# Performance work log

Measured on AMD Instinct MI355X. Metric: run time of the kernel, lower is better.

## Reference

```python
import jax, jax.numpy as jnp
import numpy as np

N, E = 50000, 250000
SD, VM = 128, 64          # scalar channels, vector multiplicity (irreps: 128x0e + 64x1e)
EA, SH = 64, 4            # edge_attr dim, spherical-harmonics dim (1x0e + 1x1e)
H, FC = 16, 256
HD = FC // H              # head dim = 16
EPS = 1e-5


def _split(x):
    return x[:, :SD], x[:, SD:].reshape(-1, VM, 3)


def _ln(s, V):
    # equivariant layer norm: standardize scalars; RMS-normalize vector norms
    s = (s - s.mean(-1, keepdims=True)) * jax.lax.rsqrt(s.var(-1, keepdims=True) + EPS)
    vn = jax.lax.rsqrt(jnp.mean(jnp.sum(V * V, -1), -1, keepdims=True) + EPS)
    return s, V * vn[..., None]


def setup_inputs() -> dict:
    key = jax.random.key(0)
    ks = iter(jax.random.split(key, 48))
    rn = lambda shp, sc=1.0: jax.random.normal(next(ks), shp, dtype=jnp.float32) * sc
    w = lambda i, o: rn((i, o), 1.0 / np.sqrt(i))
    z = lambda d: jnp.zeros((d,), jnp.float32)
    return dict(
        node_features=rn((N, SD + 3 * VM)),
        edge_attr=rn((E, EA)),
        edge_sh=rn((E, SH)),
        Wq=w(SD, FC), bq=z(FC),
        Wk=w(SD, FC), bk=z(FC),
        We=w(EA, FC), be=z(FC),
        Wv_s=w(SD, SD), bv_s=z(SD), Wv_v=w(VM, VM),
        w_ss=w(SD, SD), w_vv_s=w(VM, SD), w_ssg=w(SD, VM), w_vvg=w(VM, VM),
        b_ms=z(SD), b_mg=z(VM),
        w_sv=w(SD, VM), w_vs=w(VM, VM), w_vvv=w(VM, VM),
        Wo_s=w(SD, SD), bo_s=z(SD), Wo_v=w(VM, VM),
        W1_s=w(SD, SD + VM), b1_s=z(SD + VM), W1_v=w(VM, VM),
        W2_s=w(SD, SD), b2_s=z(SD), W2_v=w(VM, VM),
        edge_index=jax.random.randint(next(ks), (2, E), 0, N, dtype=jnp.int32),
        batch=jnp.zeros((N,), jnp.int32),
    )


def reference(node_features, edge_attr, edge_sh, Wq, bq, Wk, bk, We, be,
              Wv_s, bv_s, Wv_v, w_ss, w_vv_s, w_ssg, w_vvg, b_ms, b_mg,
              w_sv, w_vs, w_vvv, Wo_s, bo_s, Wo_v,
              W1_s, b1_s, W1_v, W2_s, b2_s, W2_v, edge_index, batch):
    src, dst = edge_index[0], edge_index[1]
    ns, nV = _split(node_features)                        # [N,SD], [N,VM,3]

    # per-edge multi-head attention scores (gathered q/k + edge bias term)
    q = (ns[dst] @ Wq + bq).reshape(-1, H, HD)
    k = (ns[src] @ Wk + bk).reshape(-1, H, HD)
    ef = (edge_attr @ We + be).reshape(-1, H, HD)
    scores = ((q * k).sum(-1) + (q * ef).sum(-1)) / np.sqrt(HD)   # [E,H]

    # per-destination-node softmax (replaces the python unique(dst) loop)
    m = jax.ops.segment_max(scores, dst, num_segments=N)
    ex = jnp.exp(scores - m[dst])
    den = jax.ops.segment_sum(ex, dst, num_segments=N)
    attn = (ex / den[dst]).mean(-1, keepdims=True)                # [E,1]

    # v projection (o3.Linear) on source nodes
    vs = ns[src] @ Wv_s + bv_s                                    # [E,SD]
    Vv = jnp.einsum('evk,vu->euk', nV[src], Wv_v)                 # [E,VM,3]

    # message MLP: fully-connected tensor product with edge SH, norm, swish-gate
    shs, shv = edge_sh[:, 0], edge_sh[:, 1:4]
    s_in = vs * shs[:, None]                                      # 0e x 0e -> 0e
    dots = jnp.einsum('evk,ek->ev', Vv, shv)                      # 1e x 1e -> 0e
    ms = s_in @ w_ss + dots @ w_vv_s + b_ms                       # [E,SD] scalars
    mg = s_in @ w_ssg + dots @ w_vvg + b_mg                       # [E,VM] gates
    MV = ((vs @ w_sv)[:, :, None] * shv[:, None, :]               # 0e x 1e -> 1e
          + jnp.einsum('evk,vu->euk', Vv * shs[:, None, None], w_vs)   # 1e x 0e -> 1e
          + jnp.einsum('evk,vu->euk', jnp.cross(Vv, shv[:, None, :]), w_vvv))  # 1e x 1e -> 1e
    sg, MVn = _ln(jnp.concatenate([ms, mg], -1), MV)
    msg_s = jax.nn.silu(sg[:, :SD])
    msg_V = MVn * jax.nn.sigmoid(sg[:, SD:])[:, :, None]

    # attention-weighted scatter-sum aggregation to destination nodes
    agg_s = jax.ops.segment_sum(msg_s * attn, dst, num_segments=N)
    agg_V = jax.ops.segment_sum(msg_V * attn[:, :, None], dst, num_segments=N)

    # out projection + residual + norm1
    x_s = ns + (agg_s @ Wo_s + bo_s)
    x_V = nV + jnp.einsum('nvk,vu->nuk', agg_V, Wo_v)
    x_s, x_V = _ln(x_s, x_V)

    # gated equivariant FFN + residual + norm2
    f = x_s @ W1_s + b1_s                                         # [N,SD+VM]
    fV = jnp.einsum('nvk,vu->nuk', x_V, W1_v)
    gV = fV * jax.nn.sigmoid(f[:, SD:])[:, :, None]
    o_s = x_s + (jax.nn.silu(f[:, :SD]) @ W2_s + b2_s)
    o_V = x_V + jnp.einsum('nvk,vu->nuk', gV, W2_v)
    o_s, o_V = _ln(o_s, o_V)
    return jnp.concatenate([o_s, o_V.reshape(-1, 3 * VM)], -1)
```

## Files before the change

### kernel.cpp

```cpp
#include <hip/hip_runtime.h>
#include <hip/hip_bf16.h>

#define NNODE 50000
#define NEDGE 250000

typedef __hip_bfloat16 bf16;
typedef __attribute__((ext_vector_type(8))) short short8v;
typedef __attribute__((ext_vector_type(4))) float f32x4;

__device__ __forceinline__ float b2f(bf16 x){ return __bfloat162float(x); }
__device__ __forceinline__ bf16  f2b(float x){ return __float2bfloat16(x); }
__device__ __forceinline__ short f2s(float x){ bf16 h=f2b(x); short s; __builtin_memcpy(&s,&h,2); return s; }
__device__ __forceinline__ float s2f(short s){ bf16 h; __builtin_memcpy(&h,&s,2); return b2f(h); }
__device__ __forceinline__ float sigm(float x){ return 1.0f/(1.0f+__expf(-x)); }
__device__ __forceinline__ float wred64(float v){
  #pragma unroll
  for(int o=32;o>0;o>>=1) v+=__shfl_xor(v,o,64);
  return v;
}
__device__ __forceinline__ float gred16(float v){
  v+=__shfl_xor(v,1,64); v+=__shfl_xor(v,2,64); v+=__shfl_xor(v,4,64); v+=__shfl_xor(v,8,64);
  return v;
}
__device__ __forceinline__ int fragOff(int r, int k){
  int kt=k>>5, k32=k&31, half=k32>>4, g=(k32&15)>>2, j=k32&3;
  return (kt<<10)+((r+(g<<4))<<4)+(half<<3)+(j<<1);
}
__device__ __forceinline__ short8v pack8(float4 a, float4 b){
  short8v s; s[0]=f2s(a.x);s[1]=f2s(a.y);s[2]=f2s(a.z);s[3]=f2s(a.w);
  s[4]=f2s(b.x);s[5]=f2s(b.y);s[6]=f2s(b.z);s[7]=f2s(b.w); return s;
}
__device__ __forceinline__ short8v pack8s(short4 a, short4 b){
  short8v s; s[0]=a.x;s[1]=a.y;s[2]=a.z;s[3]=a.w;s[4]=b.x;s[5]=b.y;s[6]=b.z;s[7]=b.w; return s;
}

#define T_WOS 0
#define T_WOV 32
#define T_W1S 40
#define T_W1V 88
#define T_W2S 96
#define T_W2V 128
#define T_WE  136
#define T_WQ  168
#define T_WK  232
#define T_WVS 296
#define T_WSS 328
#define T_WSSG 360
#define T_WSV 376
#define T_WVV 392
#define T_WVVS 400
#define T_WVVG 416
#define T_WVS2 424
#define T_WVVV 432
#define T_TOT 440

__global__ __launch_bounds__(64) void k_prep(
  const float* __restrict__ Wo_s, const float* __restrict__ Wo_v,
  const float* __restrict__ W1_s, const float* __restrict__ W1_v,
  const float* __restrict__ W2_s, const float* __restrict__ W2_v,
  const float* __restrict__ WeM,
  const float* __restrict__ Wq, const float* __restrict__ Wk,
  const float* __restrict__ Wv_s,
  const float* __restrict__ w_ss, const float* __restrict__ w_ssg,
  const float* __restrict__ w_sv,
  const float* __restrict__ Wv_v, const float* __restrict__ w_vv_s,
  const float* __restrict__ w_vvg, const float* __restrict__ w_vs,
  const float* __restrict__ w_vvv,
  short* __restrict__ P)
{
  const int T=blockIdx.x, l=threadIdx.x;
  const float* W; int N, KT, lt;
  if(T<T_WOV){ W=Wo_s; N=128; KT=4; lt=T; }
  else if(T<T_W1S){ W=Wo_v; N=64; KT=2; lt=T-T_WOV; }
  else if(T<T_W1V){ W=W1_s; N=192; KT=4; lt=T-T_W1S; }
  else if(T<T_W2S){ W=W1_v; N=64; KT=2; lt=T-T_W1V; }
  else if(T<T_W2V){ W=W2_s; N=128; KT=4; lt=T-T_W2S; }
  else if(T<T_WE){ W=W2_v; N=64; KT=2; lt=T-T_W2V; }
  else if(T<T_WQ){ W=WeM; N=256; KT=2; lt=T-T_WE; }
  else if(T<T_WK){ W=Wq; N=256; KT=4; lt=T-T_WQ; }
  else if(T<T_WVS){ W=Wk; N=256; KT=4; lt=T-T_WK; }
  else if(T<T_WSS){ W=Wv_s; N=128; KT=4; lt=T-T_WVS; }
  else if(T<T_WSSG){ W=w_ss; N=128; KT=4; lt=T-T_WSS; }
  else if(T<T_WSV){ W=w_ssg; N=64; KT=4; lt=T-T_WSSG; }
  else if(T<T_WVV){ W=w_sv; N=64; KT=4; lt=T-T_WSV; }
  else if(T<T_WVVS){ W=Wv_v; N=64; KT=2; lt=T-T_WVV; }
  else if(T<T_WVVG){ W=w_vv_s; N=128; KT=2; lt=T-T_WVVS; }
  else if(T<T_WVS2){ W=w_vvg; N=64; KT=2; lt=T-T_WVVG; }
  else if(T<T_WVVV){ W=w_vs; N=64; KT=2; lt=T-T_WVS2; }
  else { W=w_vvv; N=64; KT=2; lt=T-T_WVVV; }
  const int nt=lt/KT, kt=lt-nt*KT;
  const int col=nt*16+(l&15);
  short8v o;
  #pragma unroll
  for(int j=0;j<8;j++){
    int k=kt*32+((j>>2)<<4)+((l>>4)<<2)+(j&3);
    o[j]=f2s(W[(size_t)k*N+col]);
  }
  *(short8v*)(P+((size_t)T<<9)+(l<<3))=o;
}


__global__ __launch_bounds__(256) void k1_mfma(
  const float* __restrict__ nf, const short* __restrict__ P,
  const float* __restrict__ bq, const float* __restrict__ bk,
  const float* __restrict__ bvs,
  bf16* __restrict__ Q, bf16* __restrict__ K, short* __restrict__ NREC2)
{
  __shared__ __align__(16) short nsF[4*512];
  __shared__ __align__(16) short vsF[4*512];
  const int t=threadIdx.x, l=t&63, w=t>>6;
  const int n0=blockIdx.x*16;
  for(int i=t;i<512;i+=256){
    int r=i>>5, c=(i&31)<<2;
    const float4 v=*(const float4*)&nf[(size_t)(n0+r)*320+c];
    short4 s; s.x=f2s(v.x); s.y=f2s(v.y); s.z=f2s(v.z); s.w=f2s(v.w);
    *(short4*)((char*)nsF+fragOff(r,c))=s;
  }
  __syncthreads();
  short8v a[4];
  #pragma unroll
  for(int kt=0;kt<4;kt++) a[kt]=*(const short8v*)((const char*)nsF+(kt<<10)+(l<<4));
  #pragma unroll
  for(int ii=0;ii<4;ii++){
    int nt=w+(ii<<2);
    f32x4 accq={0.f,0.f,0.f,0.f}, acck={0.f,0.f,0.f,0.f};
    #pragma unroll
    for(int kt=0;kt<4;kt++){
      short8v bq8=*(const short8v*)(P+(((size_t)(T_WQ+nt*4+kt))<<9)+(l<<3));
      short8v bk8=*(const short8v*)(P+(((size_t)(T_WK+nt*4+kt))<<9)+(l<<3));
      accq=__builtin_amdgcn_mfma_f32_16x16x32_bf16(a[kt],bq8,accq,0,0,0);
      acck=__builtin_amdgcn_mfma_f32_16x16x32_bf16(a[kt],bk8,acck,0,0,0);
    }
    int col=(nt<<4)+(l&15);
    float bqs=bq[col], bks=bk[col];
    #pragma unroll
    for(int r=0;r<4;r++){
      int row=((l>>4)<<2)+r;
      Q[(size_t)(n0+row)*256+col]=f2b(accq[r]+bqs);
      K[(size_t)(n0+row)*256+col]=f2b(acck[r]+bks);
    }
  }
  #pragma unroll
  for(int ii=0;ii<2;ii++){
    int nt=w+(ii<<2);
    f32x4 acc={0.f,0.f,0.f,0.f};
    #pragma unroll
    for(int kt=0;kt<4;kt++){
      short8v b=*(const short8v*)(P+(((size_t)(T_WVS+nt*4+kt))<<9)+(l<<3));
      acc=__builtin_amdgcn_mfma_f32_16x16x32_bf16(a[kt],b,acc,0,0,0);
    }
    int col=(nt<<4)+(l&15);
    float bv=bvs[col];
    #pragma unroll
    for(int r=0;r<4;r++){
      int row=((l>>4)<<2)+r;
      *(short*)((char*)vsF+fragOff(row,col))=f2s(acc[r]+bv);
    }
  }
  __syncthreads();
  #pragma unroll
  for(int kt=0;kt<4;kt++) a[kt]=*(const short8v*)((const char*)vsF+(kt<<10)+(l<<4));
  #pragma unroll
  for(int ii=0;ii<4;ii++){
    int nt=w+(ii<<2);
    int bt;
    if(nt<8) bt=T_WSS+nt*4;
    else if(nt<12) bt=T_WSSG+(nt-8)*4;
    else bt=T_WSV+(nt-12)*4;
    f32x4 acc={0.f,0.f,0.f,0.f};
    #pragma unroll
    for(int kt=0;kt<4;kt++){
      short8v b=*(const short8v*)(P+(((size_t)(bt+kt))<<9)+(l<<3));
      acc=__builtin_amdgcn_mfma_f32_16x16x32_bf16(a[kt],b,acc,0,0,0);
    }
    int col=(nt<<4)+(l&15);
    int lane, sslot;
    if(nt<8){ lane=col&63; sslot=(col>=64)?1:0; }
    else if(nt<12){ lane=col-128; sslot=2; }
    else { lane=col-192; sslot=3; }
    #pragma unroll
    for(int r=0;r<4;r++){
      int row=((l>>4)<<2)+r;
      NREC2[(size_t)(n0+row)*1280 + (lane<<2) + sslot]=f2s(acc[r]);
    }
  }
}

__global__ __launch_bounds__(256) void k2_mfma(
  const float* __restrict__ nf, const short* __restrict__ P,
  short* __restrict__ NREC2)
{
  __shared__ __align__(16) short nvF[6*512];
  __shared__ __align__(16) short vvF[6*512];
  const int t=threadIdx.x, l=t&63, w=t>>6;
  const int n0=blockIdx.x*16;
  for(int i=t;i<3072;i+=256){
    int r=i/192, c=i-r*192;
    int v=c/3, k=c-3*v;
    float x=nf[(size_t)(n0+r)*320+128+c];
    *(short*)((char*)nvF+(k<<11)+fragOff(r,v))=f2s(x);
  }
  __syncthreads();
  #pragma unroll
  for(int jj=0;jj<3;jj++){
    int job=w+(jj<<2);
    int p=job>>2, nt=job&3;
    f32x4 acc={0.f,0.f,0.f,0.f};
    #pragma unroll
    for(int kt=0;kt<2;kt++){
      short8v a2=*(const short8v*)((const char*)nvF+(p<<11)+(kt<<10)+(l<<4));
      short8v b=*(const short8v*)(P+(((size_t)(T_WVV+nt*2+kt))<<9)+(l<<3));
      acc=__builtin_amdgcn_mfma_f32_16x16x32_bf16(a2,b,acc,0,0,0);
    }
    int col=(nt<<4)+(l&15);
    #pragma unroll
    for(int r=0;r<4;r++){
      int row=((l>>4)<<2)+r;
      *(short*)((char*)vvF+(p<<11)+fragOff(row,col))=f2s(acc[r]);
    }
  }
  __syncthreads();
  #pragma unroll
  for(int jj=0;jj<15;jj++){
    int job=w+(jj<<2);
    int p=job/20, r20=job-p*20;
    int nt, bt, G0;
    if(r20<8){ nt=r20; bt=T_WVVS+nt*2; G0=0; }
    else if(r20<12){ nt=r20-8; bt=T_WVVG+nt*2; G0=1; }
    else if(r20<16){ nt=r20-12; bt=T_WVS2+nt*2; G0=2; }
    else { nt=r20-16; bt=T_WVVV+nt*2; G0=3; }
    f32x4 acc={0.f,0.f,0.f,0.f};
    #pragma unroll
    for(int kt=0;kt<2;kt++){
      short8v a2=*(const short8v*)((const char*)vvF+(p<<11)+(kt<<10)+(l<<4));
      short8v b=*(const short8v*)(P+(((size_t)(bt+kt))<<9)+(l<<3));
      acc=__builtin_amdgcn_mfma_f32_16x16x32_bf16(a2,b,acc,0,0,0);
    }
    int col=(nt<<4)+(l&15);
    int G;
    if(G0==0)      G = p*2 + (col>=64 ? 1 : 0);
    else if(G0==1) G = 6 + p;
    else if(G0==2) G = 9 + p;
    else           G = 12 + p;
    int lane = col & 63;
    int addr = ((1+(G>>2))<<8) + (lane<<2) + (G&3);
    #pragma unroll
    for(int r=0;r<4;r++){
      int row=((l>>4)<<2)+r;
      NREC2[(size_t)(n0+row)*1280 + addr]=f2s(acc[r]);
    }
  }
}

__global__ __launch_bounds__(256) void k_hist(const int* __restrict__ eidx, int* __restrict__ counts){
  int e=blockIdx.x*256+threadIdx.x;
  if(e<NEDGE) atomicAdd(&counts[eidx[NEDGE+e]],1);
}

__global__ __launch_bounds__(1024) void k_scan(const int* __restrict__ counts, int* __restrict__ off, int* __restrict__ cursor){
  __shared__ int wsum[16];
  __shared__ int woff[17];
  __shared__ int carry_s;
  const int t=threadIdx.x, ln=t&63, wid=t>>6;
  if(t==0) carry_s=0;
  __syncthreads();
  for(int base=0;base<NNODE;base+=1024){
    int idx=base+t;
    int v=(idx<NNODE)?counts[idx]:0;
    int incl=v;
    #pragma unroll
    for(int o=1;o<64;o<<=1){ int x=__shfl_up(incl,o,64); if(ln>=o) incl+=x; }
    if(ln==63) wsum[wid]=incl;
    __syncthreads();
    if(t<16){
      int s=wsum[t];
      #pragma unroll
      for(int o=1;o<16;o<<=1){ int x=__shfl_up(s,o,64); if(t>=o) s+=x; }
      woff[t+1]=s;
      if(t==0) woff[0]=0;
    }
    __syncthreads();
    int excl=carry_s+woff[wid]+(incl-v);
    if(idx<NNODE){ off[idx]=excl; cursor[idx]=excl; }
    __syncthreads();
    if(t==0) carry_s+=woff[16];
    __syncthreads();
  }
  if(t==0) off[NNODE]=NEDGE;
}

__global__ __launch_bounds__(256) void k_scatter(const int* __restrict__ eidx, int* __restrict__ cursor, int* __restrict__ eord){
  int e=blockIdx.x*256+threadIdx.x;
  if(e<NEDGE){
    int d=eidx[NEDGE+e];
    int pos=atomicAdd(&cursor[d],1);
    eord[pos]=e;
  }
}

__global__ __launch_bounds__(256) void k3_mfma(
  const float* __restrict__ eattr, const int* __restrict__ eidx,
  const short* __restrict__ P, const float* __restrict__ be,
  const bf16* __restrict__ Q, const bf16* __restrict__ K,
  float* __restrict__ SC)
{
  __shared__ __align__(16) short aeF[2*512];
  __shared__ __align__(16) float ef[16][260];
  __shared__ int ssrc[16], sdst[16];
  const int t=threadIdx.x, l=t&63, w=t>>6;
  const int e0=blockIdx.x*16;
  if(t<16){ ssrc[t]=eidx[e0+t]; sdst[t]=eidx[NEDGE+e0+t]; }
  {
    int r=t>>4, c4=(t&15)<<2;
    const float4 v=*(const float4*)&eattr[(size_t)(e0+r)*64+c4];
    short4 s; s.x=f2s(v.x); s.y=f2s(v.y); s.z=f2s(v.z); s.w=f2s(v.w);
    *(short4*)((char*)aeF+fragOff(r,c4))=s;
  }
  __syncthreads();
  {
    short8v a0=*(const short8v*)((const char*)aeF+(l<<4));
    short8v a1=*(const short8v*)((const char*)aeF+1024+(l<<4));
    #pragma unroll
    for(int ii=0;ii<4;ii++){
      int nt=w+(ii<<2);
      f32x4 acc={0.f,0.f,0.f,0.f};
      short8v b0=*(const short8v*)(P+(((size_t)(T_WE+nt*2+0))<<9)+(l<<3));
      short8v b1=*(const short8v*)(P+(((size_t)(T_WE+nt*2+1))<<9)+(l<<3));
      acc=__builtin_amdgcn_mfma_f32_16x16x32_bf16(a0,b0,acc,0,0,0);
      acc=__builtin_amdgcn_mfma_f32_16x16x32_bf16(a1,b1,acc,0,0,0);
      int col=(nt<<4)+(l&15);
      float bv=be[col];
      #pragma unroll
      for(int r=0;r<4;r++){ int row=((l>>4)<<2)+r; ef[row][col]=acc[r]+bv; }
    }
  }
  __syncthreads();
  {
    const int h=l&15, qt=l>>4;
    const int ch=h*16+(qt<<2);
    #pragma unroll
    for(int j=0;j<4;j++){
      int el=w*4+j;
      int s=ssrc[el], d=sdst[el];
      short4 qs=*(const short4*)((const short*)Q+(size_t)d*256+ch);
      short4 ks=*(const short4*)((const short*)K+(size_t)s*256+ch);
      const float4 e4=*(const float4*)&ef[el][ch];
      float p = s2f(qs.x)*(s2f(ks.x)+e4.x)
              + s2f(qs.y)*(s2f(ks.y)+e4.y)
              + s2f(qs.z)*(s2f(ks.z)+e4.z)
              + s2f(qs.w)*(s2f(ks.w)+e4.w);
      p += __shfl_xor(p,16,64);
      p += __shfl_xor(p,32,64);
      if(qt==0) SC[(size_t)(e0+el)*16+h]=p*0.25f;
    }
  }
}

__global__ __launch_bounds__(256) void k5_att(
  const float* __restrict__ SC, const int* __restrict__ OFF,
  const int* __restrict__ EORD, float* __restrict__ ATT)
{
  const int l=threadIdx.x&63;
  const int n=blockIdx.x*4+(threadIdx.x>>6);
  const int beg=OFF[n], end=OFF[n+1];
  const int j=l>>4, h=l&15;
  float mh=-1e30f;
  for(int i=beg+j;i<end;i+=4) mh=fmaxf(mh, SC[(size_t)EORD[i]*16+h]);
  mh=fmaxf(mh,__shfl_xor(mh,16,64));
  mh=fmaxf(mh,__shfl_xor(mh,32,64));
  float dh=0.f;
  for(int i=beg+j;i<end;i+=4) dh+=__expf(SC[(size_t)EORD[i]*16+h]-mh);
  dh+=__shfl_xor(dh,16,64);
  dh+=__shfl_xor(dh,32,64);
  float rdh=(end>beg)?1.f/dh:0.f;
  for(int i0=beg;i0<end;i0+=4){
    int i=i0+j;
    int e=0; float a=0.f; bool act=(i<end);
    if(act){ e=EORD[i]; a=__expf(SC[(size_t)e*16+h]-mh)*rdh; }
    a=gred16(a);
    if(h==0 && act) ATT[e]=a*(1.f/16.f);
  }
}

__global__ __launch_bounds__(256) void k6_agg(
  const int* __restrict__ eidx, const float* __restrict__ esh,
  const short* __restrict__ NREC2, const float* __restrict__ ATT,
  const int* __restrict__ OFF, const int* __restrict__ EORD,
  const float* __restrict__ b_ms, const float* __restrict__ b_mg,
  float* __restrict__ AGS, float* __restrict__ AGV)
{
  const int l = threadIdx.x & 63;
  const int n = blockIdx.x*4 + (threadIdx.x>>6);
  const int beg=OFF[n], end=OFF[n+1];
  const float bmsa=b_ms[l], bmsb=b_ms[64+l], bmgv=b_mg[l];

  float as0=0.f,as1=0.f,av0acc=0.f,av1acc=0.f,av2acc=0.f;
  for(int i=beg;i<end;i++){
    const int e=EORD[i];
    const int s=eidx[e];
    const float att=ATT[e];
    const float4 sh4=*(const float4*)&esh[(size_t)e*4];
    const float shs=sh4.x, sh0=sh4.y, sh1=sh4.z, sh2=sh4.w;

    const short* R = NREC2 + (size_t)s*1280 + (l<<2);
    const short4 q0=*(const short4*)(R);
    const short4 q1=*(const short4*)(R+256);
    const short4 q2=*(const short4*)(R+512);
    const short4 q3=*(const short4*)(R+768);
    const short4 q4=*(const short4*)(R+1024);

    float msa = shs*s2f(q0.x) + s2f(q1.x)*sh0 + s2f(q1.z)*sh1 + s2f(q2.x)*sh2 + bmsa;
    float msb = shs*s2f(q0.y) + s2f(q1.y)*sh0 + s2f(q1.w)*sh1 + s2f(q2.y)*sh2 + bmsb;
    float mgv = shs*s2f(q0.z) + s2f(q2.z)*sh0 + s2f(q2.w)*sh1 + s2f(q3.x)*sh2 + bmgv;

    float sum = wred64(msa+msb+mgv);
    float sq  = wred64(msa*msa+msb*msb+mgv*mgv);
    float mean = sum*(1.f/192.f);
    float var  = sq*(1.f/192.f) - mean*mean;
    float rs   = rsqrtf(var + 1e-5f);

    const float svv=s2f(q0.w);
    const float w0=s2f(q3.y), w1=s2f(q3.z), w2=s2f(q3.w);
    const float c0=s2f(q4.x), c1=s2f(q4.y), c2=s2f(q4.z);
    float cr0 = c1*sh2 - c2*sh1;
    float cr1 = c2*sh0 - c0*sh2;
    float cr2 = c0*sh1 - c1*sh0;
    float mv0 = svv*sh0 + shs*w0 + cr0;
    float mv1 = svv*sh1 + shs*w1 + cr1;
    float mv2 = svv*sh2 + shs*w2 + cr2;
    float vsq = wred64(mv0*mv0+mv1*mv1+mv2*mv2);
    float vn  = rsqrtf(vsq*(1.f/64.f) + 1e-5f);

    float sga=(msa-mean)*rs, sgb=(msb-mean)*rs, sgg=(mgv-mean)*rs;
    float wV = vn * sigm(sgg) * att;
    as0 += sga*sigm(sga)*att;
    as1 += sgb*sigm(sgb)*att;
    av0acc += mv0*wV;
    av1acc += mv1*wV;
    av2acc += mv2*wV;
  }
  AGS[(size_t)n*128+l]     =as0;
  AGS[(size_t)n*128+64+l]  =as1;
  AGV[(size_t)n*192+l]     =av0acc;
  AGV[(size_t)n*192+64+l]  =av1acc;
  AGV[(size_t)n*192+128+l] =av2acc;
}

__global__ __launch_bounds__(256) void k7_mfma(
  const float* __restrict__ nf,
  const float* __restrict__ AGS, const float* __restrict__ AGV,
  const short* __restrict__ P,
  const float* __restrict__ bo_s, const float* __restrict__ b1_s, const float* __restrict__ b2_s,
  float* __restrict__ out)
{
  __shared__ float xs[16][132];
  __shared__ float xv[16][196];
  __shared__ short ffh[16][204];
  __shared__ __align__(16) short asA[4*512];
  __shared__ __align__(16) short avA[6*512];
  __shared__ float smean[16], srs[16], svn[16];
  const int t=threadIdx.x, l=t&63, w=t>>6;
  const int n0=blockIdx.x*16;
  const int lam=t&63, kt4=t>>6;
  const int fr=lam&15, fg=lam>>4;

  for(int i=t;i<2048;i+=256){ int r=i>>7,c=i&127; xs[r][c]=nf[(size_t)(n0+r)*320+c]; }
  for(int i=t;i<3072;i+=256){ int r=i/192,cc=i-r*192; int k=cc>>6,u=cc&63; xv[r][cc]=nf[(size_t)(n0+r)*320+128+u*3+k]; }
  {
    const float* base=&AGS[(size_t)(n0+fr)*128 + (kt4<<5) + (fg<<2)];
    float4 va=*(const float4*)base, vb=*(const float4*)(base+16);
    *(short8v*)((char*)asA+(kt4<<10)+(lam<<4))=pack8(va,vb);
  }
  for(int i=t;i<384;i+=256){
    int seg=i>>6, lm=i&63, r=lm&15, g=lm>>4;
    int p=seg>>1, k2=seg&1;
    const float* base=&AGV[(size_t)(n0+r)*192 + (p<<6) + (k2<<5) + (g<<2)];
    float4 va=*(const float4*)base, vb=*(const float4*)(base+16);
    *(short8v*)((char*)avA+(seg<<10)+(lm<<4))=pack8(va,vb);
  }
  __syncthreads();

  {
    short8v a[4];
    #pragma unroll
    for(int kt=0;kt<4;kt++) a[kt]=*(const short8v*)((const char*)asA+(kt<<10)+(l<<4));
    #pragma unroll
    for(int ii=0;ii<2;ii++){
      int nt=w+(ii<<2);
      f32x4 acc={0.f,0.f,0.f,0.f};
      #pragma unroll
      for(int kt=0;kt<4;kt++){
        short8v b=*(const short8v*)(P+(((size_t)(T_WOS+nt*4+kt))<<9)+(l<<3));
        acc=__builtin_amdgcn_mfma_f32_16x16x32_bf16(a[kt],b,acc,0,0,0);
      }
      int col=(nt<<4)+(l&15);
      float bv=bo_s[col];
      #pragma unroll
      for(int r=0;r<4;r++){ int row=((l>>4)<<2)+r; xs[row][col]+=acc[r]+bv; }
    }
    #pragma unroll
    for(int ii=0;ii<3;ii++){
      int tid=w*3+ii, p=tid>>2, nt2=tid&3;
      f32x4 acc={0.f,0.f,0.f,0.f};
      #pragma unroll
      for(int kt=0;kt<2;kt++){
        short8v a2=*(const short8v*)((const char*)avA+(((p<<1)+kt)<<10)+(l<<4));
        short8v b=*(const short8v*)(P+(((size_t)(T_WOV+nt2*2+kt))<<9)+(l<<3));
        acc=__builtin_amdgcn_mfma_f32_16x16x32_bf16(a2,b,acc,0,0,0);
      }
      int col=(p<<6)+(nt2<<4)+(l&15);
      #pragma unroll
      for(int r=0;r<4;r++){ int row=((l>>4)<<2)+r; xv[row][col]+=acc[r]; }
    }
  }
  __syncthreads();

  {
    const int nn=t>>4, g=t&15;
    float sum=0,sq=0;
    #pragma unroll
    for(int j=0;j<8;j++){ float x=xs[nn][g+16*j]; sum+=x; sq+=x*x; }
    sum=gred16(sum); sq=gred16(sq);
    float mean=sum*(1.f/128.f);
    float var=sq*(1.f/128.f)-mean*mean;
    float vsq=0;
    #pragma unroll
    for(int j=0;j<12;j++){ float x=xv[nn][g+16*j]; vsq+=x*x; }
    vsq=gred16(vsq);
    if(g==0){ smean[nn]=mean; srs[nn]=rsqrtf(var+1e-5f); svn[nn]=rsqrtf(vsq*(1.f/64.f)+1e-5f); }
  }
  __syncthreads();

  for(int i=t;i<512;i+=256){
    int r=i>>5, c=(i&31)<<2;
    float m=smean[r], rs=srs[r];
    float4 v=*(float4*)&xs[r][c];
    v.x=(v.x-m)*rs; v.y=(v.y-m)*rs; v.z=(v.z-m)*rs; v.w=(v.w-m)*rs;
    *(float4*)&xs[r][c]=v;
  }
  for(int i=t;i<768;i+=256){
    int r=i/48, c=(i-r*48)<<2;
    float vn=svn[r];
    float4 v=*(float4*)&xv[r][c];
    v.x*=vn; v.y*=vn; v.z*=vn; v.w*=vn;
    *(float4*)&xv[r][c]=v;
  }
  __syncthreads();
  {
    float4 va=*(const float4*)&xs[fr][(kt4<<5)+(fg<<2)];
    float4 vb=*(const float4*)&xs[fr][(kt4<<5)+16+(fg<<2)];
    *(short8v*)((char*)asA+(kt4<<10)+(lam<<4))=pack8(va,vb);
  }
  for(int i=t;i<384;i+=256){
    int seg=i>>6, lm=i&63, r=lm&15, g=lm>>4;
    int p=seg>>1, k2=seg&1;
    float4 va=*(const float4*)&xv[r][(p<<6)+(k2<<5)+(g<<2)];
    float4 vb=*(const float4*)&xv[r][(p<<6)+(k2<<5)+16+(g<<2)];
    *(short8v*)((char*)avA+(seg<<10)+(lm<<4))=pack8(va,vb);
  }
  __syncthreads();

  {
    short8v a[4];
    #pragma unroll
    for(int kt=0;kt<4;kt++) a[kt]=*(const short8v*)((const char*)asA+(kt<<10)+(l<<4));
    #pragma unroll
    for(int ii=0;ii<3;ii++){
      int nt=w+(ii<<2);
      f32x4 acc={0.f,0.f,0.f,0.f};
      #pragma unroll
      for(int kt=0;kt<4;kt++){
        short8v b=*(const short8v*)(P+(((size_t)(T_W1S+nt*4+kt))<<9)+(l<<3));
        acc=__builtin_amdgcn_mfma_f32_16x16x32_bf16(a[kt],b,acc,0,0,0);
      }
      int col=(nt<<4)+(l&15);
      float bv=b1_s[col];
      #pragma unroll
      for(int r=0;r<4;r++){ int row=((l>>4)<<2)+r; ffh[row][col]=f2s(acc[r]+bv); }
    }
  }
  __syncthreads();

  f32x4 g4acc[3];
  {
    #pragma unroll
    for(int ii=0;ii<3;ii++){
      int tid=w*3+ii, p=tid>>2, nt2=tid&3;
      f32x4 acc={0.f,0.f,0.f,0.f};
      #pragma unroll
      for(int kt=0;kt<2;kt++){
        short8v a2=*(const short8v*)((const char*)avA+(((p<<1)+kt)<<10)+(l<<4));
        short8v b=*(const short8v*)(P+(((size_t)(T_W1V+nt2*2+kt))<<9)+(l<<3));
        acc=__builtin_amdgcn_mfma_f32_16x16x32_bf16(a2,b,acc,0,0,0);
      }
      g4acc[ii]=acc;
    }
    for(int i=t;i<512;i+=256){
      int r=i>>5, c=(i&31)<<2;
      short4 sv4=*(short4*)&ffh[r][c];
      float x0=s2f(sv4.x), x1=s2f(sv4.y), x2=s2f(sv4.z), x3=s2f(sv4.w);
      sv4.x=f2s(x0*sigm(x0)); sv4.y=f2s(x1*sigm(x1)); sv4.z=f2s(x2*sigm(x2)); sv4.w=f2s(x3*sigm(x3));
      *(short4*)&ffh[r][c]=sv4;
    }
  }
  __syncthreads();

  {
    short4 sa=*(const short4*)&ffh[fr][(kt4<<5)+(fg<<2)];
    short4 sb=*(const short4*)&ffh[fr][(kt4<<5)+16+(fg<<2)];
    *(short8v*)((char*)asA+(kt4<<10)+(lam<<4))=pack8s(sa,sb);
  }
  {
    #pragma unroll
    for(int ii=0;ii<3;ii++){
      int tid=w*3+ii, nt2=tid&3;
      int uu=(nt2<<4)+(l&15);
      #pragma unroll
      for(int r=0;r<4;r++){
        int row=((l>>4)<<2)+r;
        g4acc[ii][r]*=sigm(s2f(ffh[row][128+uu]));
      }
    }
  }
  __syncthreads();

  {
    #pragma unroll
    for(int ii=0;ii<3;ii++){
      int tid=w*3+ii, p=tid>>2, nt2=tid&3;
      int uu=(nt2<<4)+(l&15);
      #pragma unroll
      for(int r=0;r<4;r++){
        int row=((l>>4)<<2)+r;
        ffh[row][(p<<6)+uu]=f2s(g4acc[ii][r]);
      }
    }
  }
  __syncthreads();
  for(int i=t;i<384;i+=256){
    int seg=i>>6, lm=i&63, r=lm&15, g=lm>>4;
    int p=seg>>1, k2=seg&1;
    short4 sa=*(const short4*)&ffh[r][(p<<6)+(k2<<5)+(g<<2)];
    short4 sb=*(const short4*)&ffh[r][(p<<6)+(k2<<5)+16+(g<<2)];
    *(short8v*)((char*)avA+(seg<<10)+(lm<<4))=pack8s(sa,sb);
  }
  __syncthreads();

  {
    short8v a[4];
    #pragma unroll
    for(int kt=0;kt<4;kt++) a[kt]=*(const short8v*)((const char*)asA+(kt<<10)+(l<<4));
    #pragma unroll
    for(int ii=0;ii<2;ii++){
      int nt=w+(ii<<2);
      f32x4 acc={0.f,0.f,0.f,0.f};
      #pragma unroll
      for(int kt=0;kt<4;kt++){
        short8v b=*(const short8v*)(P+(((size_t)(T_W2S+nt*4+kt))<<9)+(l<<3));
        acc=__builtin_amdgcn_mfma_f32_16x16x32_bf16(a[kt],b,acc,0,0,0);
      }
      int col=(nt<<4)+(l&15);
      float bv=b2_s[col];
      #pragma unroll
      for(int r=0;r<4;r++){ int row=((l>>4)<<2)+r; xs[row][col]+=acc[r]+bv; }
    }
    #pragma unroll
    for(int ii=0;ii<3;ii++){
      int tid=w*3+ii, p=tid>>2, nt2=tid&3;
      f32x4 acc={0.f,0.f,0.f,0.f};
      #pragma unroll
      for(int kt=0;kt<2;kt++){
        short8v a2=*(const short8v*)((const char*)avA+(((p<<1)+kt)<<10)+(l<<4));
        short8v b=*(const short8v*)(P+(((size_t)(T_W2V+nt2*2+kt))<<9)+(l<<3));
        acc=__builtin_amdgcn_mfma_f32_16x16x32_bf16(a2,b,acc,0,0,0);
      }
      int col=(p<<6)+(nt2<<4)+(l&15);
      #pragma unroll
      for(int r=0;r<4;r++){ int row=((l>>4)<<2)+r; xv[row][col]+=acc[r]; }
    }
  }
  __syncthreads();

  {
    const int nn=t>>4, g=t&15;
    float sum=0,sq=0;
    #pragma unroll
    for(int j=0;j<8;j++){ float x=xs[nn][g+16*j]; sum+=x; sq+=x*x; }
    sum=gred16(sum); sq=gred16(sq);
    float mean=sum*(1.f/128.f);
    float var=sq*(1.f/128.f)-mean*mean;
    float vsq=0;
    #pragma unroll
    for(int j=0;j<12;j++){ float x=xv[nn][g+16*j]; vsq+=x*x; }
    vsq=gred16(vsq);
    if(g==0){ smean[nn]=mean; srs[nn]=rsqrtf(var+1e-5f); svn[nn]=rsqrtf(vsq*(1.f/64.f)+1e-5f); }
  }
  __syncthreads();

  for(int i=t;i<16*320;i+=256){
    int nn=i/320, c=i-nn*320;
    float v;
    if(c<128) v=(xs[nn][c]-smean[nn])*srs[nn];
    else { int j=c-128; int u=j/3, k=j-u*3; v=xv[nn][(k<<6)+u]*svn[nn]; }
    out[(size_t)(n0+nn)*320+c]=v;
  }
}

extern "C" void kernel_launch(void* const* d_in, const int* in_sizes, int n_in,
                              void* d_out, int out_size, void* d_ws, size_t ws_size,
                              hipStream_t stream)
{
  (void)in_sizes; (void)n_in; (void)out_size; (void)ws_size;
  const float* nf    =(const float*)d_in[0];
  const float* eattr =(const float*)d_in[1];
  const float* esh   =(const float*)d_in[2];
  const float* Wq    =(const float*)d_in[3];  const float* bq  =(const float*)d_in[4];
  const float* Wk    =(const float*)d_in[5];  const float* bk  =(const float*)d_in[6];
  const float* We    =(const float*)d_in[7];  const float* be  =(const float*)d_in[8];
  const float* Wv_s  =(const float*)d_in[9];  const float* bv_s=(const float*)d_in[10];
  const float* Wv_v  =(const float*)d_in[11];
  const float* w_ss  =(const float*)d_in[12]; const float* w_vv_s=(const float*)d_in[13];
  const float* w_ssg =(const float*)d_in[14]; const float* w_vvg =(const float*)d_in[15];
  const float* b_ms  =(const float*)d_in[16]; const float* b_mg  =(const float*)d_in[17];
  const float* w_sv  =(const float*)d_in[18]; const float* w_vs  =(const float*)d_in[19];
  const float* w_vvv =(const float*)d_in[20];
  const float* Wo_s  =(const float*)d_in[21]; const float* bo_s  =(const float*)d_in[22];
  const float* Wo_v  =(const float*)d_in[23];
  const float* W1_s  =(const float*)d_in[24]; const float* b1_s  =(const float*)d_in[25];
  const float* W1_v  =(const float*)d_in[26];
  const float* W2_s  =(const float*)d_in[27]; const float* b2_s  =(const float*)d_in[28];
  const float* W2_v  =(const float*)d_in[29];
  const int*   eidx  =(const int*)d_in[30];
  float* out=(float*)d_out;

  char* w=(char*)d_ws;
  bf16* Q    =(bf16*)w;  w+=(size_t)NNODE*256*2;
  bf16* Kb   =(bf16*)w;  w+=(size_t)NNODE*256*2;
  short* NREC2=(short*)w; w+=(size_t)NNODE*1280*2;
  float* SC  =(float*)w; w+=(size_t)NEDGE*16*4;
  float* ATT =(float*)w; w+=(size_t)NEDGE*4;
  float* AGS =(float*)w; w+=(size_t)NNODE*128*4;
  float* AGV =(float*)w; w+=(size_t)NNODE*192*4;
  short* P   =(short*)w; w+=(size_t)T_TOT*512*2;
  int* COUNTS=(int*)w;   w+=(size_t)NNODE*4;
  int* OFFb  =(int*)w;   w+=(size_t)(NNODE+1)*4;
  int* CURSOR=(int*)w;   w+=(size_t)NNODE*4;
  int* EORDb =(int*)w;   w+=(size_t)NEDGE*4;

  hipMemsetAsync(COUNTS,0,(size_t)NNODE*4,stream);

  k_prep    <<<T_TOT,64,0,stream>>>(Wo_s,Wo_v,W1_s,W1_v,W2_s,W2_v,We,
                                    Wq,Wk,Wv_s,w_ss,w_ssg,w_sv,
                                    Wv_v,w_vv_s,w_vvg,w_vs,w_vvv,P);
  k_hist    <<<(NEDGE+255)/256,256,0,stream>>>(eidx,COUNTS);
  k_scan    <<<1,1024,0,stream>>>(COUNTS,OFFb,CURSOR);
  k_scatter <<<(NEDGE+255)/256,256,0,stream>>>(eidx,CURSOR,EORDb);
  k1_mfma   <<<NNODE/16,256,0,stream>>>(nf,P,bq,bk,bv_s,Q,Kb,NREC2);
  k2_mfma   <<<NNODE/16,256,0,stream>>>(nf,P,NREC2);
  k3_mfma   <<<NEDGE/16,256,0,stream>>>(eattr,eidx,P,be,Q,Kb,SC);
  k5_att    <<<NNODE/4,256,0,stream>>>(SC,OFFb,EORDb,ATT);
  k6_agg    <<<NNODE/4,256,0,stream>>>(eidx,esh,NREC2,ATT,OFFb,EORDb,b_ms,b_mg,AGS,AGV);
  k7_mfma   <<<NNODE/16,256,0,stream>>>(nf,AGS,AGV,P,bo_s,b1_s,b2_s,out);
}
```

Baseline: 513.2 us.

## Fuse softmax into aggregation, fold histogram into edge-score kernel, prefetch gathers

The destination-degree histogram moves into the edge-score kernel, which removes the separate k_hist launch. The softmax normalisation is fused into the aggregation kernel: per-edge attention weights are computed in chunks of 64 into shared memory, so the ATT buffer and the k5 launch go away. The aggregation loop also software-prefetches the next edge's gathered node record and spherical harmonics to hide gather latency. The cost is higher register pressure and more sequential work inside each wave.

```diff
diff --git a/kernel.cpp b/kernel.cpp
--- a/kernel.cpp
+++ b/kernel.cpp
@@ -252,11 +252,6 @@
   }
 }
 
-__global__ __launch_bounds__(256) void k_hist(const int* __restrict__ eidx, int* __restrict__ counts){
-  int e=blockIdx.x*256+threadIdx.x;
-  if(e<NEDGE) atomicAdd(&counts[eidx[NEDGE+e]],1);
-}
-
 __global__ __launch_bounds__(1024) void k_scan(const int* __restrict__ counts, int* __restrict__ off, int* __restrict__ cursor){
   __shared__ int wsum[16];
   __shared__ int woff[17];
@@ -302,14 +297,19 @@
   const float* __restrict__ eattr, const int* __restrict__ eidx,
   const short* __restrict__ P, const float* __restrict__ be,
   const bf16* __restrict__ Q, const bf16* __restrict__ K,
-  float* __restrict__ SC)
+  float* __restrict__ SC, int* __restrict__ counts)
 {
   __shared__ __align__(16) short aeF[2*512];
   __shared__ __align__(16) float ef[16][260];
   __shared__ int ssrc[16], sdst[16];
   const int t=threadIdx.x, l=t&63, w=t>>6;
   const int e0=blockIdx.x*16;
-  if(t<16){ ssrc[t]=eidx[e0+t]; sdst[t]=eidx[NEDGE+e0+t]; }
+  if(t<16){
+    ssrc[t]=eidx[e0+t];
+    int d=eidx[NEDGE+e0+t];
+    sdst[t]=d;
+    atomicAdd(&counts[d],1);
+  }
   {
     int r=t>>4, c4=(t&15)<<2;
     const float4 v=*(const float4*)&eattr[(size_t)(e0+r)*64+c4];
@@ -356,14 +356,21 @@
   }
 }
 
-__global__ __launch_bounds__(256) void k5_att(
-  const float* __restrict__ SC, const int* __restrict__ OFF,
-  const int* __restrict__ EORD, float* __restrict__ ATT)
+__global__ __launch_bounds__(256) void k6_agg(
+  const int* __restrict__ eidx, const float* __restrict__ esh,
+  const short* __restrict__ NREC2, const float* __restrict__ SC,
+  const int* __restrict__ OFF, const int* __restrict__ EORD,
+  const float* __restrict__ b_ms, const float* __restrict__ b_mg,
+  float* __restrict__ AGS, float* __restrict__ AGV)
 {
-  const int l=threadIdx.x&63;
-  const int n=blockIdx.x*4+(threadIdx.x>>6);
+  __shared__ float att_s[4][64];
+  const int l = threadIdx.x & 63;
+  const int wid = threadIdx.x>>6;
+  const int n = blockIdx.x*4 + wid;
   const int beg=OFF[n], end=OFF[n+1];
+  const float bmsa=b_ms[l], bmsb=b_ms[64+l], bmgv=b_mg[l];
   const int j=l>>4, h=l&15;
+
   float mh=-1e30f;
   for(int i=beg+j;i<end;i+=4) mh=fmaxf(mh, SC[(size_t)EORD[i]*16+h]);
   mh=fmaxf(mh,__shfl_xor(mh,16,64));
@@ -372,72 +379,69 @@
   for(int i=beg+j;i<end;i+=4) dh+=__expf(SC[(size_t)EORD[i]*16+h]-mh);
   dh+=__shfl_xor(dh,16,64);
   dh+=__shfl_xor(dh,32,64);
-  float rdh=(end>beg)?1.f/dh:0.f;
-  for(int i0=beg;i0<end;i0+=4){
-    int i=i0+j;
-    int e=0; float a=0.f; bool act=(i<end);
-    if(act){ e=EORD[i]; a=__expf(SC[(size_t)e*16+h]-mh)*rdh; }
-    a=gred16(a);
-    if(h==0 && act) ATT[e]=a*(1.f/16.f);
-  }
-}
-
-__global__ __launch_bounds__(256) void k6_agg(
-  const int* __restrict__ eidx, const float* __restrict__ esh,
-  const short* __restrict__ NREC2, const float* __restrict__ ATT,
-  const int* __restrict__ OFF, const int* __restrict__ EORD,
-  const float* __restrict__ b_ms, const float* __restrict__ b_mg,
-  float* __restrict__ AGS, float* __restrict__ AGV)
-{
-  const int l = threadIdx.x & 63;
-  const int n = blockIdx.x*4 + (threadIdx.x>>6);
-  const int beg=OFF[n], end=OFF[n+1];
-  const float bmsa=b_ms[l], bmsb=b_ms[64+l], bmgv=b_mg[l];
+  const float rdh=(end>beg)?1.f/dh:0.f;
 
   float as0=0.f,as1=0.f,av0acc=0.f,av1acc=0.f,av2acc=0.f;
-  for(int i=beg;i<end;i++){
-    const int e=EORD[i];
-    const int s=eidx[e];
-    const float att=ATT[e];
-    const float4 sh4=*(const float4*)&esh[(size_t)e*4];
-    const float shs=sh4.x, sh0=sh4.y, sh1=sh4.z, sh2=sh4.w;
-
-    const short* R = NREC2 + (size_t)s*1280 + (l<<2);
-    const short4 q0=*(const short4*)(R);
-    const short4 q1=*(const short4*)(R+256);
-    const short4 q2=*(const short4*)(R+512);
-    const short4 q3=*(const short4*)(R+768);
-    const short4 q4=*(const short4*)(R+1024);
-
-    float msa = shs*s2f(q0.x) + s2f(q1.x)*sh0 + s2f(q1.z)*sh1 + s2f(q2.x)*sh2 + bmsa;
-    float msb = shs*s2f(q0.y) + s2f(q1.y)*sh0 + s2f(q1.w)*sh1 + s2f(q2.y)*sh2 + bmsb;
-    float mgv = shs*s2f(q0.z) + s2f(q2.z)*sh0 + s2f(q2.w)*sh1 + s2f(q3.x)*sh2 + bmgv;
-
-    float sum = wred64(msa+msb+mgv);
-    float sq  = wred64(msa*msa+msb*msb+mgv*mgv);
-    float mean = sum*(1.f/192.f);
-    float var  = sq*(1.f/192.f) - mean*mean;
-    float rs   = rsqrtf(var + 1e-5f);
-
-    const float svv=s2f(q0.w);
-    const float w0=s2f(q3.y), w1=s2f(q3.z), w2=s2f(q3.w);
-    const float c0=s2f(q4.x), c1=s2f(q4.y), c2=s2f(q4.z);
-    float cr0 = c1*sh2 - c2*sh1;
-    float cr1 = c2*sh0 - c0*sh2;
-    float cr2 = c0*sh1 - c1*sh0;
-    float mv0 = svv*sh0 + shs*w0 + cr0;
-    float mv1 = svv*sh1 + shs*w1 + cr1;
-    float mv2 = svv*sh2 + shs*w2 + cr2;
-    float vsq = wred64(mv0*mv0+mv1*mv1+mv2*mv2);
-    float vn  = rsqrtf(vsq*(1.f/64.f) + 1e-5f);
-
-    float sga=(msa-mean)*rs, sgb=(msb-mean)*rs, sgg=(mgv-mean)*rs;
-    float wV = vn * sigm(sgg) * att;
-    as0 += sga*sigm(sga)*att;
-    as1 += sgb*sigm(sgb)*att;
-    av0acc += mv0*wV;
-    av1acc += mv1*wV;
-    av2acc += mv2*wV;
+
+  for(int cb=beg; cb<end; cb+=64){
+    const int ce = (cb+64<end)? cb+64 : end;
+    for(int i0=cb;i0<ce;i0+=4){
+      int i=i0+j; bool act=(i<ce);
+      float a = act ? __expf(SC[(size_t)EORD[i]*16+h]-mh)*rdh : 0.f;
+      a=gred16(a);
+      if(h==0&&act) att_s[wid][i-cb]=a*(1.f/16.f);
+    }
+    int e=EORD[cb], s=eidx[e];
+    const short* R=NREC2+(size_t)s*1280+(l<<2);
+    short4 q0=*(const short4*)(R),     q1=*(const short4*)(R+256);
+    short4 q2=*(const short4*)(R+512), q3=*(const short4*)(R+768);
+    short4 q4=*(const short4*)(R+1024);
+    float4 sh4=*(const float4*)&esh[(size_t)e*4];
+
+    for(int i=cb;i<ce;i++){
+      const short4 p0=q0,p1=q1,p2=q2,p3=q3,p4=q4;
+      const float4 ps=sh4;
+      if(i+1<ce){
+        int e2=EORD[i+1], s2=eidx[e2];
+        const short* R2=NREC2+(size_t)s2*1280+(l<<2);
+        q0=*(const short4*)(R2);     q1=*(const short4*)(R2+256);
+        q2=*(const short4*)(R2+512); q3=*(const short4*)(R2+768);
+        q4=*(const short4*)(R2+1024);
+        sh4=*(const float4*)&esh[(size_t)e2*4];
+      }
+      const float att=att_s[wid][i-cb];
+      const float shs=ps.x, sh0=ps.y, sh1=ps.z, sh2=ps.w;
+
+      float msa = shs*s2f(p0.x) + s2f(p1.x)*sh0 + s2f(p1.z)*sh1 + s2f(p2.x)*sh2 + bmsa;
+      float msb = shs*s2f(p0.y) + s2f(p1.y)*sh0 + s2f(p1.w)*sh1 + s2f(p2.y)*sh2 + bmsb;
+      float mgv = shs*s2f(p0.z) + s2f(p2.z)*sh0 + s2f(p2.w)*sh1 + s2f(p3.x)*sh2 + bmgv;
+
+      float sum = wred64(msa+msb+mgv);
+      float sq  = wred64(msa*msa+msb*msb+mgv*mgv);
+      float mean = sum*(1.f/192.f);
+      float var  = sq*(1.f/192.f) - mean*mean;
+      float rs   = rsqrtf(var + 1e-5f);
+
+      const float svv=s2f(p0.w);
+      const float w0=s2f(p3.y), w1=s2f(p3.z), w2=s2f(p3.w);
+      const float c0=s2f(p4.x), c1=s2f(p4.y), c2=s2f(p4.z);
+      float cr0 = c1*sh2 - c2*sh1;
+      float cr1 = c2*sh0 - c0*sh2;
+      float cr2 = c0*sh1 - c1*sh0;
+      float mv0 = svv*sh0 + shs*w0 + cr0;
+      float mv1 = svv*sh1 + shs*w1 + cr1;
+      float mv2 = svv*sh2 + shs*w2 + cr2;
+      float vsq = wred64(mv0*mv0+mv1*mv1+mv2*mv2);
+      float vn  = rsqrtf(vsq*(1.f/64.f) + 1e-5f);
+
+      float sga=(msa-mean)*rs, sgb=(msb-mean)*rs, sgg=(mgv-mean)*rs;
+      float wV = vn * sigm(sgg) * att;
+      as0 += sga*sigm(sga)*att;
+      as1 += sgb*sigm(sgb)*att;
+      av0acc += mv0*wV;
+      av1acc += mv1*wV;
+      av2acc += mv2*wV;
+    }
   }
   AGS[(size_t)n*128+l]     =as0;
   AGS[(size_t)n*128+64+l]  =as1;
@@ -738,7 +742,6 @@
   bf16* Kb   =(bf16*)w;  w+=(size_t)NNODE*256*2;
   short* NREC2=(short*)w; w+=(size_t)NNODE*1280*2;
   float* SC  =(float*)w; w+=(size_t)NEDGE*16*4;
-  float* ATT =(float*)w; w+=(size_t)NEDGE*4;
   float* AGS =(float*)w; w+=(size_t)NNODE*128*4;
   float* AGV =(float*)w; w+=(size_t)NNODE*192*4;
   short* P   =(short*)w; w+=(size_t)T_TOT*512*2;
@@ -752,13 +755,11 @@
   k_prep    <<<T_TOT,64,0,stream>>>(Wo_s,Wo_v,W1_s,W1_v,W2_s,W2_v,We,
                                     Wq,Wk,Wv_s,w_ss,w_ssg,w_sv,
                                     Wv_v,w_vv_s,w_vvg,w_vs,w_vvv,P);
-  k_hist    <<<(NEDGE+255)/256,256,0,stream>>>(eidx,COUNTS);
+  k1_mfma   <<<NNODE/16,256,0,stream>>>(nf,P,bq,bk,bv_s,Q,Kb,NREC2);
+  k2_mfma   <<<NNODE/16,256,0,stream>>>(nf,P,NREC2);
+  k3_mfma   <<<NEDGE/16,256,0,stream>>>(eattr,eidx,P,be,Q,Kb,SC,COUNTS);
   k_scan    <<<1,1024,0,stream>>>(COUNTS,OFFb,CURSOR);
   k_scatter <<<(NEDGE+255)/256,256,0,stream>>>(eidx,CURSOR,EORDb);
-  k1_mfma   <<<NNODE/16,256,0,stream>>>(nf,P,bq,bk,bv_s,Q,Kb,NREC2);
-  k2_mfma   <<<NNODE/16,256,0,stream>>>(nf,P,NREC2);
-  k3_mfma   <<<NEDGE/16,256,0,stream>>>(eattr,eidx,P,be,Q,Kb,SC);
-  k5_att    <<<NNODE/4,256,0,stream>>>(SC,OFFb,EORDb,ATT);
-  k6_agg    <<<NNODE/4,256,0,stream>>>(eidx,esh,NREC2,ATT,OFFb,EORDb,b_ms,b_mg,AGS,AGV);
+  k6_agg    <<<NNODE/4,256,0,stream>>>(eidx,esh,NREC2,SC,OFFb,EORDb,b_ms,b_mg,AGS,AGV);
   k7_mfma   <<<NNODE/16,256,0,stream>>>(nf,AGS,AGV,P,bo_s,b1_s,b2_s,out);
 }
```

New measurement: 542.8 us. 1.06x slower.

## Parallelize CSR scan, fuse histogram into k3, and store edge data in sorted order

Applied to the files above, without the earlier changes.

The single-block serial scan over 50000 nodes becomes a three-kernel multi-block scan. The destination histogram moves into k3's edge loop, so the separate k_hist pass disappears. k_scatter now also writes source ids and spherical harmonics in destination-sorted order, and k5 writes attention in sorted order. This lets k6 read contiguously instead of doing indirect EORD gathers. The cost is extra workspace, two more small launches, and additional scatter writes.

```diff
diff --git a/kernel.cpp b/kernel.cpp
--- a/kernel.cpp
+++ b/kernel.cpp
@@ -20,6 +20,11 @@
 }
 __device__ __forceinline__ float gred16(float v){
   v+=__shfl_xor(v,1,64); v+=__shfl_xor(v,2,64); v+=__shfl_xor(v,4,64); v+=__shfl_xor(v,8,64);
+  return v;
+}
+__device__ __forceinline__ int ired64(int v){
+  #pragma unroll
+  for(int o=32;o>0;o>>=1) v+=__shfl_xor(v,o,64);
   return v;
 }
 __device__ __forceinline__ int fragOff(int r, int k){
@@ -252,49 +257,64 @@
   }
 }
 
-__global__ __launch_bounds__(256) void k_hist(const int* __restrict__ eidx, int* __restrict__ counts){
-  int e=blockIdx.x*256+threadIdx.x;
-  if(e<NEDGE) atomicAdd(&counts[eidx[NEDGE+e]],1);
-}
-
-__global__ __launch_bounds__(1024) void k_scan(const int* __restrict__ counts, int* __restrict__ off, int* __restrict__ cursor){
-  __shared__ int wsum[16];
-  __shared__ int woff[17];
-  __shared__ int carry_s;
+#define SCAN_NB 196
+
+__global__ __launch_bounds__(256) void k_scan1(const int* __restrict__ counts, int* __restrict__ bsum){
   const int t=threadIdx.x, ln=t&63, wid=t>>6;
-  if(t==0) carry_s=0;
-  __syncthreads();
-  for(int base=0;base<NNODE;base+=1024){
-    int idx=base+t;
-    int v=(idx<NNODE)?counts[idx]:0;
-    int incl=v;
-    #pragma unroll
-    for(int o=1;o<64;o<<=1){ int x=__shfl_up(incl,o,64); if(ln>=o) incl+=x; }
-    if(ln==63) wsum[wid]=incl;
-    __syncthreads();
-    if(t<16){
-      int s=wsum[t];
-      #pragma unroll
-      for(int o=1;o<16;o<<=1){ int x=__shfl_up(s,o,64); if(t>=o) s+=x; }
-      woff[t+1]=s;
-      if(t==0) woff[0]=0;
-    }
-    __syncthreads();
-    int excl=carry_s+woff[wid]+(incl-v);
-    if(idx<NNODE){ off[idx]=excl; cursor[idx]=excl; }
-    __syncthreads();
-    if(t==0) carry_s+=woff[16];
-    __syncthreads();
-  }
-  if(t==0) off[NNODE]=NEDGE;
-}
-
-__global__ __launch_bounds__(256) void k_scatter(const int* __restrict__ eidx, int* __restrict__ cursor, int* __restrict__ eord){
+  int idx=blockIdx.x*256+t;
+  int v=(idx<NNODE)?counts[idx]:0;
+  int s=ired64(v);
+  __shared__ int ws[4];
+  if(ln==0) ws[wid]=s;
+  __syncthreads();
+  if(t==0) bsum[blockIdx.x]=ws[0]+ws[1]+ws[2]+ws[3];
+}
+
+__global__ __launch_bounds__(256) void k_scan2(const int* __restrict__ bsum, int* __restrict__ boff){
+  const int t=threadIdx.x, ln=t&63, wid=t>>6;
+  int v=(t<SCAN_NB)?bsum[t]:0;
+  int incl=v;
+  #pragma unroll
+  for(int o=1;o<64;o<<=1){ int x=__shfl_up(incl,o,64); if(ln>=o) incl+=x; }
+  __shared__ int wtot[4], wpre[4];
+  if(ln==63) wtot[wid]=incl;
+  __syncthreads();
+  if(t==0){ int s=0; for(int k=0;k<4;k++){ wpre[k]=s; s+=wtot[k]; } }
+  __syncthreads();
+  if(t<SCAN_NB) boff[t]=wpre[wid]+incl-v;
+}
+
+__global__ __launch_bounds__(256) void k_scan3(const int* __restrict__ counts, const int* __restrict__ boff,
+                                               int* __restrict__ off, int* __restrict__ cursor){
+  const int t=threadIdx.x, ln=t&63, wid=t>>6;
+  int idx=blockIdx.x*256+t;
+  int v=(idx<NNODE)?counts[idx]:0;
+  int incl=v;
+  #pragma unroll
+  for(int o=1;o<64;o<<=1){ int x=__shfl_up(incl,o,64); if(ln>=o) incl+=x; }
+  __shared__ int wtot[4], wpre[4];
+  if(ln==63) wtot[wid]=incl;
+  __syncthreads();
+  if(t==0){ int s=0; for(int k=0;k<4;k++){ wpre[k]=s; s+=wtot[k]; } }
+  __syncthreads();
+  int excl=boff[blockIdx.x]+wpre[wid]+incl-v;
+  if(idx<NNODE){ off[idx]=excl; cursor[idx]=excl; }
+  if(idx==NNODE) off[NNODE]=NEDGE;
+  if(blockIdx.x==SCAN_NB-1 && t==255) off[NNODE]=NEDGE;
+}
+
+__global__ __launch_bounds__(256) void k_scatter(
+  const int* __restrict__ eidx, const float* __restrict__ esh,
+  int* __restrict__ cursor, int* __restrict__ eord,
+  int* __restrict__ srcs, float* __restrict__ eshs)
+{
   int e=blockIdx.x*256+threadIdx.x;
   if(e<NEDGE){
     int d=eidx[NEDGE+e];
     int pos=atomicAdd(&cursor[d],1);
     eord[pos]=e;
+    srcs[pos]=eidx[e];
+    *(float4*)&eshs[(size_t)pos*4]=*(const float4*)&esh[(size_t)e*4];
   }
 }
 
@@ -302,14 +322,19 @@
   const float* __restrict__ eattr, const int* __restrict__ eidx,
   const short* __restrict__ P, const float* __restrict__ be,
   const bf16* __restrict__ Q, const bf16* __restrict__ K,
-  float* __restrict__ SC)
+  float* __restrict__ SC, int* __restrict__ counts)
 {
   __shared__ __align__(16) short aeF[2*512];
   __shared__ __align__(16) float ef[16][260];
   __shared__ int ssrc[16], sdst[16];
   const int t=threadIdx.x, l=t&63, w=t>>6;
   const int e0=blockIdx.x*16;
-  if(t<16){ ssrc[t]=eidx[e0+t]; sdst[t]=eidx[NEDGE+e0+t]; }
+  if(t<16){
+    ssrc[t]=eidx[e0+t];
+    int d=eidx[NEDGE+e0+t];
+    sdst[t]=d;
+    atomicAdd(&counts[d],1);
+  }
   {
     int r=t>>4, c4=(t&15)<<2;
     const float4 v=*(const float4*)&eattr[(size_t)(e0+r)*64+c4];
@@ -358,7 +383,7 @@
 
 __global__ __launch_bounds__(256) void k5_att(
   const float* __restrict__ SC, const int* __restrict__ OFF,
-  const int* __restrict__ EORD, float* __restrict__ ATT)
+  const int* __restrict__ EORD, float* __restrict__ ATTs)
 {
   const int l=threadIdx.x&63;
   const int n=blockIdx.x*4+(threadIdx.x>>6);
@@ -375,17 +400,17 @@
   float rdh=(end>beg)?1.f/dh:0.f;
   for(int i0=beg;i0<end;i0+=4){
     int i=i0+j;
-    int e=0; float a=0.f; bool act=(i<end);
-    if(act){ e=EORD[i]; a=__expf(SC[(size_t)e*16+h]-mh)*rdh; }
+    float a=0.f; bool act=(i<end);
+    if(act) a=__expf(SC[(size_t)EORD[i]*16+h]-mh)*rdh;
     a=gred16(a);
-    if(h==0 && act) ATT[e]=a*(1.f/16.f);
+    if(h==0 && act) ATTs[i]=a*(1.f/16.f);
   }
 }
 
 __global__ __launch_bounds__(256) void k6_agg(
-  const int* __restrict__ eidx, const float* __restrict__ esh,
-  const short* __restrict__ NREC2, const float* __restrict__ ATT,
-  const int* __restrict__ OFF, const int* __restrict__ EORD,
+  const int* __restrict__ SRCs, const float* __restrict__ ESHs,
+  const short* __restrict__ NREC2, const float* __restrict__ ATTs,
+  const int* __restrict__ OFF,
   const float* __restrict__ b_ms, const float* __restrict__ b_mg,
   float* __restrict__ AGS, float* __restrict__ AGV)
 {
@@ -396,10 +421,9 @@
 
   float as0=0.f,as1=0.f,av0acc=0.f,av1acc=0.f,av2acc=0.f;
   for(int i=beg;i<end;i++){
-    const int e=EORD[i];
-    const int s=eidx[e];
-    const float att=ATT[e];
-    const float4 sh4=*(const float4*)&esh[(size_t)e*4];
+    const int s=SRCs[i];
+    const float att=ATTs[i];
+    const float4 sh4=*(const float4*)&ESHs[(size_t)i*4];
     const float shs=sh4.x, sh0=sh4.y, sh1=sh4.z, sh2=sh4.w;
 
     const short* R = NREC2 + (size_t)s*1280 + (l<<2);
@@ -738,7 +762,8 @@
   bf16* Kb   =(bf16*)w;  w+=(size_t)NNODE*256*2;
   short* NREC2=(short*)w; w+=(size_t)NNODE*1280*2;
   float* SC  =(float*)w; w+=(size_t)NEDGE*16*4;
-  float* ATT =(float*)w; w+=(size_t)NEDGE*4;
+  float* ESHs=(float*)w; w+=(size_t)NEDGE*4*4;
+  float* ATTs=(float*)w; w+=(size_t)NEDGE*4;
   float* AGS =(float*)w; w+=(size_t)NNODE*128*4;
   float* AGV =(float*)w; w+=(size_t)NNODE*192*4;
   short* P   =(short*)w; w+=(size_t)T_TOT*512*2;
@@ -746,19 +771,23 @@
   int* OFFb  =(int*)w;   w+=(size_t)(NNODE+1)*4;
   int* CURSOR=(int*)w;   w+=(size_t)NNODE*4;
   int* EORDb =(int*)w;   w+=(size_t)NEDGE*4;
+  int* SRCs  =(int*)w;   w+=(size_t)NEDGE*4;
+  int* BSUM  =(int*)w;   w+=(size_t)256*4;
+  int* BOFF  =(int*)w;   w+=(size_t)256*4;
 
   hipMemsetAsync(COUNTS,0,(size_t)NNODE*4,stream);
 
   k_prep    <<<T_TOT,64,0,stream>>>(Wo_s,Wo_v,W1_s,W1_v,W2_s,W2_v,We,
                                     Wq,Wk,Wv_s,w_ss,w_ssg,w_sv,
                                     Wv_v,w_vv_s,w_vvg,w_vs,w_vvv,P);
-  k_hist    <<<(NEDGE+255)/256,256,0,stream>>>(eidx,COUNTS);
-  k_scan    <<<1,1024,0,stream>>>(COUNTS,OFFb,CURSOR);
-  k_scatter <<<(NEDGE+255)/256,256,0,stream>>>(eidx,CURSOR,EORDb);
   k1_mfma   <<<NNODE/16,256,0,stream>>>(nf,P,bq,bk,bv_s,Q,Kb,NREC2);
   k2_mfma   <<<NNODE/16,256,0,stream>>>(nf,P,NREC2);
-  k3_mfma   <<<NEDGE/16,256,0,stream>>>(eattr,eidx,P,be,Q,Kb,SC);
-  k5_att    <<<NNODE/4,256,0,stream>>>(SC,OFFb,EORDb,ATT);
-  k6_agg    <<<NNODE/4,256,0,stream>>>(eidx,esh,NREC2,ATT,OFFb,EORDb,b_ms,b_mg,AGS,AGV);
+  k3_mfma   <<<NEDGE/16,256,0,stream>>>(eattr,eidx,P,be,Q,Kb,SC,COUNTS);
+  k_scan1   <<<SCAN_NB,256,0,stream>>>(COUNTS,BSUM);
+  k_scan2   <<<1,256,0,stream>>>(BSUM,BOFF);
+  k_scan3   <<<SCAN_NB,256,0,stream>>>(COUNTS,BOFF,OFFb,CURSOR);
+  k_scatter <<<(NEDGE+255)/256,256,0,stream>>>(eidx,esh,CURSOR,EORDb,SRCs,ESHs);
+  k5_att    <<<NNODE/4,256,0,stream>>>(SC,OFFb,EORDb,ATTs);
+  k6_agg    <<<NNODE/4,256,0,stream>>>(SRCs,ESHs,NREC2,ATTs,OFFb,b_ms,b_mg,AGS,AGV);
   k7_mfma   <<<NNODE/16,256,0,stream>>>(nf,AGS,AGV,P,bo_s,b1_s,b2_s,out);
 }
```

Result: faster. 459.6 us (-10.5%).
